# Kernel tuning notes

Hardware: AMD Instinct MI355X
Metric: run time of the kernel (lower is better)

## Reference

```python
import jax, jax.numpy as jnp
import numpy as np

B = 1048576
STATE_DIM, HIDDEN, LATENT = 21, 64, 14
LN_EPS = 1e-5
# index map replicating the torch repeat/cat reconstruction of metric attention (13 -> 21)
EXPAND_IDX = np.array([0, 1, 2, 3, 4, 4, 5, 5, 5, 6, 6, 6, 7, 7, 8, 9, 9, 10, 10, 11, 12])


def setup_inputs() -> dict:
    key = jax.random.key(0)
    ks = jax.random.split(key, 20)

    def w(k, shape, fan_in):
        return (jax.random.uniform(k, shape, jnp.float32, -1.0, 1.0) / np.sqrt(fan_in))

    return {
        'state': jax.random.normal(ks[0], (B, STATE_DIM), jnp.float32),
        # encoder
        'W_enc1': w(ks[1], (STATE_DIM, HIDDEN), STATE_DIM),
        'b_enc1': w(ks[2], (HIDDEN,), STATE_DIM),
        'ln_g': jnp.ones((HIDDEN,), jnp.float32),
        'ln_b': jnp.zeros((HIDDEN,), jnp.float32),
        'W_enc2': w(ks[3], (HIDDEN, HIDDEN), HIDDEN),
        'b_enc2': w(ks[4], (HIDDEN,), HIDDEN),
        'W_enc3': w(ks[5], (HIDDEN, LATENT), HIDDEN),
        'b_enc3': w(ks[6], (LATENT,), HIDDEN),
        # decoder
        'W_dec1': w(ks[7], (LATENT, HIDDEN), LATENT),
        'b_dec1': w(ks[8], (HIDDEN,), LATENT),
        'W_dec2': w(ks[9], (HIDDEN, 8), HIDDEN),
        'b_dec2': w(ks[10], (8,), HIDDEN),
        # attention heads
        'W_m': w(ks[11], (STATE_DIM, 13), STATE_DIM),
        'b_m': w(ks[12], (13,), STATE_DIM),
        'W_h': w(ks[13], (STATE_DIM, 6), STATE_DIM),
        'b_h': w(ks[14], (6,), STATE_DIM),
        'W_c': w(ks[15], (STATE_DIM, 4), STATE_DIM),
        'b_c': w(ks[16], (4,), STATE_DIM),
        # learnable head scales (init 1.0 as in torch)
        's_m': jnp.asarray(1.0, jnp.float32),
        's_h': jnp.asarray(1.0, jnp.float32),
        's_c': jnp.asarray(1.0, jnp.float32),
    }


def _normalize(state):
    ns = state
    ns = ns.at[:, 0:2].set(state[:, 0:2] / 3.0)
    ns = ns.at[:, 17].set(state[:, 17] / 2.0)
    ns = ns.at[:, 18].set(state[:, 18] / 4.0)
    ns = ns.at[:, 19].set(jnp.clip(state[:, 19], 0.0, 2.0) / 2.0)
    return ns


def _layernorm(x, g, b):
    mu = jnp.mean(x, axis=-1, keepdims=True)
    var = jnp.mean(jnp.square(x - mu), axis=-1, keepdims=True)
    return (x - mu) / jnp.sqrt(var + LN_EPS) * g + b


def reference(state, W_enc1, b_enc1, ln_g, ln_b, W_enc2, b_enc2, W_enc3, b_enc3,
              W_dec1, b_dec1, W_dec2, b_dec2, W_m, b_m, W_h, b_h, W_c, b_c,
              s_m, s_h, s_c):
    ns = _normalize(state)  # [B, 21]

    metric = jax.nn.softmax(ns @ W_m + b_m, axis=-1) * (jax.nn.sigmoid(s_m) * 2.0)  # [B,13]
    hyp = jax.nn.softmax(ns @ W_h + b_h, axis=-1) * (jax.nn.sigmoid(s_h) * 2.0)      # [B,6]
    curr = jax.nn.softmax(ns @ W_c + b_c, axis=-1) * (jax.nn.sigmoid(s_c) * 2.0)     # [B,4]

    attended = ns * metric[:, EXPAND_IDX]  # [B,21]

    h = jnp.tanh(_layernorm(attended @ W_enc1 + b_enc1, ln_g, ln_b))
    h = jax.nn.relu(h @ W_enc2 + b_enc2)
    latent = h @ W_enc3 + b_enc3  # [B,14]

    d = jax.nn.relu(latent @ W_dec1 + b_dec1)
    corrections = jnp.tanh(d @ W_dec2 + b_dec2)  # [B,8]

    return corrections, latent, metric, hyp, curr
```

## Files before the change

kernel.cpp:

```cpp
#include <hip/hip_runtime.h>

static constexpr int SD = 21, HD = 64, LT = 14;
static constexpr int NFRAG = 40;

typedef _Float16       f16x4  __attribute__((ext_vector_type(4)));
typedef float          f32x4  __attribute__((ext_vector_type(4)));
typedef unsigned       u32x2v __attribute__((ext_vector_type(2)));
typedef unsigned short u16x4v __attribute__((ext_vector_type(4)));
typedef __fp16         pk2    __attribute__((ext_vector_type(2)));

__device__ __forceinline__ float frcp(float x){ return __builtin_amdgcn_rcpf(x); }
__device__ __forceinline__ float frsq(float x){ return __builtin_amdgcn_rsqf(x); }

__device__ __forceinline__ void wave_fence(){
    asm volatile("s_waitcnt lgkmcnt(0)" ::: "memory");
    __builtin_amdgcn_sched_barrier(0);
}

__device__ __forceinline__ unsigned packrtz(float a, float b){
    pk2 h = __builtin_amdgcn_cvt_pkrtz(a, b);
    union { pk2 h; unsigned u; } u; u.h = h; return u.u;
}
__device__ __forceinline__ unsigned short f16bits(float v){
    _Float16 h = (_Float16)v;
    union { _Float16 h; unsigned short s; } u; u.h = h; return u.s;
}
__device__ __forceinline__ float ftanh(float x){
    x = fminf(15.0f, fmaxf(-15.0f, x));
    float e = __expf(2.0f * x);
    return (e - 1.0f) * frcp(e + 1.0f);
}
template<int NN>
__device__ __forceinline__ void softmax_scale(float (&v)[NN], float gate){
    float mx = v[0];
#pragma unroll
    for (int j = 1; j < NN; ++j) mx = fmaxf(mx, v[j]);
    float s = 0.0f;
#pragma unroll
    for (int j = 0; j < NN; ++j){ v[j] = __expf(v[j] - mx); s += v[j]; }
    float r = frcp(s) * gate;
#pragma unroll
    for (int j = 0; j < NN; ++j) v[j] *= r;
}

union Frag2 { u32x2v u2; unsigned u[2]; f16x4 f; };
union FragH { u16x4v uh; f16x4 f; };

__device__ __forceinline__ f32x4 mfma16(f16x4 a, f16x4 b, f32x4 c){
    return __builtin_amdgcn_mfma_f32_16x16x16f16(a, b, c, 0, 0, 0);
}

__device__ __forceinline__ float headsW(const float* Wm, const float* Wh,
                                        const float* Wc, int k, int j){
    if (j < 13) return Wm[k*13 + j];
    if (j < 19) return Wh[k*6 + (j - 13)];
    if (j < 23) return Wc[k*4 + (j - 19)];
    return 0.0f;
}

__global__ void pack_bfrags(const float* __restrict__ W1, const float* __restrict__ W2,
                            const float* __restrict__ W3, const float* __restrict__ Wd1,
                            const float* __restrict__ Wd2,
                            const float* __restrict__ Wm, const float* __restrict__ Wh,
                            const float* __restrict__ Wc, unsigned* __restrict__ ws)
{
    int t = blockIdx.x * blockDim.x + threadIdx.x;
    if (t >= NFRAG * 64) return;
    int fid = t >> 6, lane = t & 63;
    int g = lane >> 4, c = lane & 15;

    if (fid >= 36) {
        int e = fid - 36, ks16 = e >> 1, ct = e & 1;
        int col = ct*16 + c;
#pragma unroll
        for (int j = 0; j < 2; ++j) {
            int k0 = ks16*16 + g*4 + 2*j;
            float a = (k0     < SD && col < 23) ? headsW(Wm, Wh, Wc, k0,   col) : 0.0f;
            float b = (k0 + 1 < SD && col < 23) ? headsW(Wm, Wh, Wc, k0+1, col) : 0.0f;
            ws[fid*128 + lane*2 + j] = packrtz(a, b);
        }
        return;
    }

    const float* W; int ks16, ct, K, Ncol, ld;
    if (fid < 8)       { W = W1;  ks16 = fid >> 2;    ct = fid & 3;  K = 21; Ncol = 64; ld = 64; }
    else if (fid < 24) { int e = fid - 8;
                         W = W2;  ks16 = e >> 2;      ct = e & 3;    K = 64; Ncol = 64; ld = 64; }
    else if (fid < 28) { W = W3;  ks16 = fid - 24;    ct = 0;        K = 64; Ncol = 14; ld = 14; }
    else if (fid < 32) { W = Wd1; ks16 = 0;           ct = fid - 28; K = 14; Ncol = 64; ld = 64; }
    else               { W = Wd2; ks16 = fid - 32;    ct = 0;        K = 64; Ncol = 8;  ld = 8;  }
    int col = ct*16 + c;
#pragma unroll
    for (int j = 0; j < 2; ++j) {
        int k0 = ks16*16 + g*4 + 2*j;
        float a = (k0     < K && col < Ncol) ? W[k0*ld + col]     : 0.0f;
        float b = (k0 + 1 < K && col < Ncol) ? W[(k0+1)*ld + col] : 0.0f;
        ws[fid*128 + lane*2 + j] = packrtz(a, b);
    }
}

__global__ __launch_bounds__(256) void statenet_mfma7(
    const float* __restrict__ state,
    const unsigned* __restrict__ pw,
    const float* __restrict__ b1,
    const float* __restrict__ lng, const float* __restrict__ lnb,
    const float* __restrict__ b2,  const float* __restrict__ b3,
    const float* __restrict__ bd1, const float* __restrict__ bd2,
    const float* __restrict__ bm,  const float* __restrict__ bh,
    const float* __restrict__ bc,
    const float* __restrict__ psm, const float* __restrict__ psh,
    const float* __restrict__ psc,
    float* __restrict__ out, int N)
{
    __shared__ __align__(16) unsigned s_buf[4*1152];
    __shared__ __align__(16) float    s_lg[4*832];

    const int tid = threadIdx.x;
    const int w  = tid >> 6, l = tid & 63;
    const int cl = l & 15,  g = l >> 4;
    const long long rowbase = (long long)blockIdx.x * 128 + w * 32;

    unsigned*       at  = s_buf + w * 1152;
    unsigned short* hb  = reinterpret_cast<unsigned short*>(s_buf) + w * 2304;
    float*          slg = s_lg + w * 832;

    const float bc0 = (cl < 13) ? bm[cl] : bh[cl - 13];
    const float bc1 = (cl < 3) ? bh[cl + 3] : ((cl < 7) ? bc[cl - 3] : 0.0f);

    float ns[SD];
    if (l < 32) {
        const long long row = rowbase + l;
        {
            const float* p = state + row * SD;
#pragma unroll
            for (int k = 0; k < SD; ++k) ns[k] = p[k];
        }
        ns[0]  *= (1.0f / 3.0f);
        ns[1]  *= (1.0f / 3.0f);
        ns[17] *= 0.5f;
        ns[18] *= 0.25f;
        ns[19]  = fminf(fmaxf(ns[19], 0.0f), 2.0f) * 0.5f;

        const int base = l * 36;
#pragma unroll
        for (int kk = 0; kk < 10; ++kk) at[base + kk] = packrtz(ns[2*kk], ns[2*kk+1]);
        at[base + 10] = packrtz(ns[20], 0.0f);
#pragma unroll
        for (int kk = 11; kk < 16; ++kk) at[base + kk] = 0u;
    }
    wave_fence();

    const u32x2v* BF2 = reinterpret_cast<const u32x2v*>(pw);
    const f32x4 vzero = {0.0f, 0.0f, 0.0f, 0.0f};
    {
        Frag2 aN[2][2];
#pragma unroll
        for (int m2 = 0; m2 < 2; ++m2)
#pragma unroll
            for (int ks = 0; ks < 2; ++ks)
                aN[m2][ks].u2 = *reinterpret_cast<const u32x2v*>(&at[(m2*16 + cl)*36 + ks*8 + 2*g]);
        f32x4 hl[2][2];
#pragma unroll
        for (int m2 = 0; m2 < 2; ++m2)
#pragma unroll
            for (int ct = 0; ct < 2; ++ct) hl[m2][ct] = vzero;
#pragma unroll
        for (int ct = 0; ct < 2; ++ct)
#pragma unroll
            for (int ks = 0; ks < 2; ++ks) {
                Frag2 bf; bf.u2 = BF2[(36 + ks*2 + ct)*64 + l];
#pragma unroll
                for (int m2 = 0; m2 < 2; ++m2)
                    hl[m2][ct] = mfma16(aN[m2][ks].f, bf.f, hl[m2][ct]);
            }
#pragma unroll
        for (int m2 = 0; m2 < 2; ++m2)
#pragma unroll
            for (int q = 0; q < 4; ++q) {
                int r = m2*16 + g*4 + q;
                slg[r*26 + cl] = hl[m2][0][q] + bc0;
                if (cl < 8) slg[r*26 + 16 + cl] = hl[m2][1][q] + bc1;
            }
    }
    wave_fence();

    if (l < 32) {
        const long long row = rowbase + l;
        float lg[24];
#pragma unroll
        for (int i = 0; i < 12; ++i) {
            float2 v = *reinterpret_cast<const float2*>(&slg[l*26 + 2*i]);
            lg[2*i] = v.x; lg[2*i+1] = v.y;
        }
        float m[13], hv[6], cv[4];
#pragma unroll
        for (int j = 0; j < 13; ++j) m[j]  = lg[j];
#pragma unroll
        for (int j = 0; j < 6;  ++j) hv[j] = lg[13 + j];
#pragma unroll
        for (int j = 0; j < 4;  ++j) cv[j] = lg[19 + j];

        const float gm = 2.0f * frcp(1.0f + __expf(-psm[0]));
        const float gh = 2.0f * frcp(1.0f + __expf(-psh[0]));
        const float gc = 2.0f * frcp(1.0f + __expf(-psc[0]));
        softmax_scale<13>(m,  gm);
        softmax_scale<6 >(hv, gh);
        softmax_scale<4 >(cv, gc);

        {
            float* pm = out + (long long)22 * N + row * 13;
#pragma unroll
            for (int j = 0; j < 13; ++j) pm[j] = m[j];
            float* ph = out + (long long)35 * N + row * 6;
#pragma unroll
            for (int j = 0; j < 3; ++j)
                reinterpret_cast<float2*>(ph)[j] = make_float2(hv[2*j], hv[2*j+1]);
            float* pc = out + (long long)41 * N + row * 4;
            reinterpret_cast<float4*>(pc)[0] = make_float4(cv[0], cv[1], cv[2], cv[3]);
        }

        constexpr int EIDX[SD] = {0,1,2,3,4,4,5,5,5,6,6,6,7,7,8,9,9,10,10,11,12};
        float atv[SD];
#pragma unroll
        for (int k = 0; k < SD; ++k) atv[k] = ns[k] * m[EIDX[k]];
        const int base = l * 36;
#pragma unroll
        for (int kk = 0; kk < 10; ++kk) at[base + kk] = packrtz(atv[2*kk], atv[2*kk+1]);
        at[base + 10] = packrtz(atv[20], 0.0f);
    }
    wave_fence();

    float b1c[4], b2c[4], bd1c[4], lgc[4], lbc[4];
#pragma unroll
    for (int t2 = 0; t2 < 4; ++t2) {
        int c2 = cl + 16*t2;
        b1c[t2] = b1[c2];  b2c[t2] = b2[c2];  bd1c[t2] = bd1[c2];
        lgc[t2] = lng[c2]; lbc[t2] = lnb[c2];
    }
    const float b3c  = (cl < 14) ? b3[cl]  : 0.0f;
    const float bd2c = (cl < 8)  ? bd2[cl] : 0.0f;

    Frag2 aA[2][2];
#pragma unroll
    for (int m2 = 0; m2 < 2; ++m2)
#pragma unroll
        for (int ks = 0; ks < 2; ++ks)
            aA[m2][ks].u2 = *reinterpret_cast<const u32x2v*>(&at[(m2*16 + cl)*36 + ks*8 + 2*g]);
    wave_fence();

    f32x4 acc[2][4];
#pragma unroll
    for (int m2 = 0; m2 < 2; ++m2)
#pragma unroll
        for (int ct = 0; ct < 4; ++ct) acc[m2][ct] = vzero;
#pragma unroll
    for (int ct = 0; ct < 4; ++ct)
#pragma unroll
        for (int ks = 0; ks < 2; ++ks) {
            Frag2 bf; bf.u2 = BF2[(ks*4 + ct)*64 + l];
#pragma unroll
            for (int m2 = 0; m2 < 2; ++m2)
                acc[m2][ct] = mfma16(aA[m2][ks].f, bf.f, acc[m2][ct]);
        }
#pragma unroll
    for (int m2 = 0; m2 < 2; ++m2) {
        float s[4], ss[4];
#pragma unroll
        for (int q = 0; q < 4; ++q) {
            float v0 = acc[m2][0][q] + b1c[0], v1 = acc[m2][1][q] + b1c[1];
            float v2 = acc[m2][2][q] + b1c[2], v3 = acc[m2][3][q] + b1c[3];
            acc[m2][0][q] = v0; acc[m2][1][q] = v1; acc[m2][2][q] = v2; acc[m2][3][q] = v3;
            s[q]  = v0 + v1 + v2 + v3;
            ss[q] = v0*v0 + v1*v1 + v2*v2 + v3*v3;
        }
#pragma unroll
        for (int q = 0; q < 4; ++q) {
#pragma unroll
            for (int d = 1; d < 16; d <<= 1) {
                s[q]  += __shfl_xor(s[q],  d, 16);
                ss[q] += __shfl_xor(ss[q], d, 16);
            }
        }
#pragma unroll
        for (int q = 0; q < 4; ++q) {
            float mu   = s[q] * (1.0f/64.0f);
            float var  = ss[q] * (1.0f/64.0f) - mu*mu;
            float istd = frsq(var + 1e-5f);
            int r = m2*16 + g*4 + q;
#pragma unroll
            for (int t2 = 0; t2 < 4; ++t2) {
                float v = ftanh(fmaf((acc[m2][t2][q] - mu) * istd, lgc[t2], lbc[t2]));
                hb[r*72 + cl + 16*t2] = f16bits(v);
            }
        }
    }
    wave_fence();

    FragH ah[2][4];
#pragma unroll
    for (int m2 = 0; m2 < 2; ++m2)
#pragma unroll
        for (int ks = 0; ks < 4; ++ks)
            ah[m2][ks].uh = *reinterpret_cast<const u16x4v*>(&hb[(m2*16 + cl)*72 + ks*16 + 4*g]);
    f32x4 a2[2][4];
#pragma unroll
    for (int m2 = 0; m2 < 2; ++m2)
#pragma unroll
        for (int ct = 0; ct < 4; ++ct) a2[m2][ct] = vzero;
#pragma unroll
    for (int ct = 0; ct < 4; ++ct)
#pragma unroll
        for (int ks = 0; ks < 4; ++ks) {
            Frag2 bf; bf.u2 = BF2[(8 + ks*4 + ct)*64 + l];
#pragma unroll
            for (int m2 = 0; m2 < 2; ++m2)
                a2[m2][ct] = mfma16(ah[m2][ks].f, bf.f, a2[m2][ct]);
        }
    wave_fence();
#pragma unroll
    for (int m2 = 0; m2 < 2; ++m2)
#pragma unroll
        for (int q = 0; q < 4; ++q) {
            int r = m2*16 + g*4 + q;
#pragma unroll
            for (int t2 = 0; t2 < 4; ++t2)
                hb[r*72 + cl + 16*t2] = f16bits(fmaxf(a2[m2][t2][q] + b2c[t2], 0.0f));
        }
    wave_fence();

#pragma unroll
    for (int m2 = 0; m2 < 2; ++m2)
#pragma unroll
        for (int ks = 0; ks < 4; ++ks)
            ah[m2][ks].uh = *reinterpret_cast<const u16x4v*>(&hb[(m2*16 + cl)*72 + ks*16 + 4*g]);
    wave_fence();
#pragma unroll
    for (int m2 = 0; m2 < 2; ++m2) {
        f32x4 a3 = vzero;
#pragma unroll
        for (int ks = 0; ks < 4; ++ks) {
            Frag2 bf; bf.u2 = BF2[(24 + ks)*64 + l];
            a3 = mfma16(ah[m2][ks].f, bf.f, a3);
        }
#pragma unroll
        for (int q = 0; q < 4; ++q) {
            float lv = a3[q] + b3c;
            int r = m2*16 + g*4 + q;
            if (cl < 14)
                out[(long long)8 * N + (rowbase + r) * 14 + cl] = lv;
            float pv = __shfl_xor(lv, 1);
            if ((cl & 1) == 0)
                at[r*36 + (cl >> 1)] = packrtz(lv, pv);
        }
    }
    wave_fence();

    Frag2 aD[2];
#pragma unroll
    for (int m2 = 0; m2 < 2; ++m2)
        aD[m2].u2 = *reinterpret_cast<const u32x2v*>(&at[(m2*16 + cl)*36 + 2*g]);
    wave_fence();
    f32x4 ad[2][4];
#pragma unroll
    for (int m2 = 0; m2 < 2; ++m2)
#pragma unroll
        for (int ct = 0; ct < 4; ++ct) ad[m2][ct] = vzero;
#pragma unroll
    for (int ct = 0; ct < 4; ++ct) {
        Frag2 bf; bf.u2 = BF2[(28 + ct)*64 + l];
#pragma unroll
        for (int m2 = 0; m2 < 2; ++m2)
            ad[m2][ct] = mfma16(aD[m2].f, bf.f, ad[m2][ct]);
    }
#pragma unroll
    for (int m2 = 0; m2 < 2; ++m2)
#pragma unroll
        for (int q = 0; q < 4; ++q) {
            int r = m2*16 + g*4 + q;
#pragma unroll
            for (int t2 = 0; t2 < 4; ++t2)
                hb[r*72 + cl + 16*t2] = f16bits(fmaxf(ad[m2][t2][q] + bd1c[t2], 0.0f));
        }
    wave_fence();

#pragma unroll
    for (int m2 = 0; m2 < 2; ++m2)
#pragma unroll
        for (int ks = 0; ks < 4; ++ks)
            ah[m2][ks].uh = *reinterpret_cast<const u16x4v*>(&hb[(m2*16 + cl)*72 + ks*16 + 4*g]);
#pragma unroll
    for (int m2 = 0; m2 < 2; ++m2) {
        f32x4 a5 = vzero;
#pragma unroll
        for (int ks = 0; ks < 4; ++ks) {
            Frag2 bf; bf.u2 = BF2[(32 + ks)*64 + l];
            a5 = mfma16(ah[m2][ks].f, bf.f, a5);
        }
#pragma unroll
        for (int q = 0; q < 4; ++q) {
            if (cl < 8)
                out[(rowbase + m2*16 + g*4 + q) * 8 + cl] = ftanh(a5[q] + bd2c);
        }
    }
}

extern "C" void kernel_launch(void* const* d_in, const int* in_sizes, int n_in,
                              void* d_out, int out_size, void* d_ws, size_t ws_size,
                              hipStream_t stream)
{
    const float* state = (const float*)d_in[0];
    const float* W1   = (const float*)d_in[1];
    const float* b1   = (const float*)d_in[2];
    const float* lng  = (const float*)d_in[3];
    const float* lnb  = (const float*)d_in[4];
    const float* W2   = (const float*)d_in[5];
    const float* b2   = (const float*)d_in[6];
    const float* W3   = (const float*)d_in[7];
    const float* b3   = (const float*)d_in[8];
    const float* Wd1  = (const float*)d_in[9];
    const float* bd1  = (const float*)d_in[10];
    const float* Wd2  = (const float*)d_in[11];
    const float* bd2  = (const float*)d_in[12];
    const float* Wm   = (const float*)d_in[13];
    const float* bm   = (const float*)d_in[14];
    const float* Wh   = (const float*)d_in[15];
    const float* bh   = (const float*)d_in[16];
    const float* Wc   = (const float*)d_in[17];
    const float* bc   = (const float*)d_in[18];
    const float* psm  = (const float*)d_in[19];
    const float* psh  = (const float*)d_in[20];
    const float* psc  = (const float*)d_in[21];

    unsigned* pw = (unsigned*)d_ws;

    hipLaunchKernelGGL(pack_bfrags, dim3((NFRAG*64 + 255)/256), dim3(256), 0, stream,
                       W1, W2, W3, Wd1, Wd2, Wm, Wh, Wc, pw);

    const int N = in_sizes[0] / SD;
    hipLaunchKernelGGL(statenet_mfma7, dim3(N / 128), dim3(256), 0, stream,
                       state, pw, b1, lng, lnb, b2, b3, bd1, bd2,
                       bm, bh, bc, psm, psh, psc,
                       (float*)d_out, N);
}
```

Before: 123.0 us.

## Chain MLP layers through MFMA accumulators via transposed products, dropping LDS staging

Swaps the operand order of each MFMA so it computes the transposed product (weights as A, activations as B). The output fragment of one layer then already has the layout of the B operand for the next layer. Hidden activations are packed to fp16 in registers and fed straight into the next MFMA, which removes the LDS write/read round trips and wave fences between encoder and decoder layers. LayerNorm reductions become two cross-group shuffles, and bias loads and output stores are vectorized. This raises register pressure and moves the head biases into the softmax thread's scalar loop.

```diff
diff --git a/kernel.cpp b/kernel.cpp
--- a/kernel.cpp
+++ b/kernel.cpp
@@ -6,7 +6,6 @@
 typedef _Float16       f16x4  __attribute__((ext_vector_type(4)));
 typedef float          f32x4  __attribute__((ext_vector_type(4)));
 typedef unsigned       u32x2v __attribute__((ext_vector_type(2)));
-typedef unsigned short u16x4v __attribute__((ext_vector_type(4)));
 typedef __fp16         pk2    __attribute__((ext_vector_type(2)));
 
 __device__ __forceinline__ float frcp(float x){ return __builtin_amdgcn_rcpf(x); }
@@ -20,10 +19,6 @@
 __device__ __forceinline__ unsigned packrtz(float a, float b){
     pk2 h = __builtin_amdgcn_cvt_pkrtz(a, b);
     union { pk2 h; unsigned u; } u; u.h = h; return u.u;
-}
-__device__ __forceinline__ unsigned short f16bits(float v){
-    _Float16 h = (_Float16)v;
-    union { _Float16 h; unsigned short s; } u; u.h = h; return u.s;
 }
 __device__ __forceinline__ float ftanh(float x){
     x = fminf(15.0f, fmaxf(-15.0f, x));
@@ -44,7 +39,6 @@
 }
 
 union Frag2 { u32x2v u2; unsigned u[2]; f16x4 f; };
-union FragH { u16x4v uh; f16x4 f; };
 
 __device__ __forceinline__ f32x4 mfma16(f16x4 a, f16x4 b, f32x4 c){
     return __builtin_amdgcn_mfma_f32_16x16x16f16(a, b, c, 0, 0, 0);
@@ -99,7 +93,7 @@
     }
 }
 
-__global__ __launch_bounds__(256) void statenet_mfma7(
+__global__ __launch_bounds__(256) void statenet_mfma8(
     const float* __restrict__ state,
     const unsigned* __restrict__ pw,
     const float* __restrict__ b1,
@@ -112,7 +106,7 @@
     const float* __restrict__ psc,
     float* __restrict__ out, int N)
 {
-    __shared__ __align__(16) unsigned s_buf[4*1152];
+    __shared__ __align__(16) unsigned s_at[4*1152];
     __shared__ __align__(16) float    s_lg[4*832];
 
     const int tid = threadIdx.x;
@@ -120,12 +114,11 @@
     const int cl = l & 15,  g = l >> 4;
     const long long rowbase = (long long)blockIdx.x * 128 + w * 32;
 
-    unsigned*       at  = s_buf + w * 1152;
-    unsigned short* hb  = reinterpret_cast<unsigned short*>(s_buf) + w * 2304;
-    float*          slg = s_lg + w * 832;
-
-    const float bc0 = (cl < 13) ? bm[cl] : bh[cl - 13];
-    const float bc1 = (cl < 3) ? bh[cl + 3] : ((cl < 7) ? bc[cl - 3] : 0.0f);
+    unsigned* at  = s_at + w * 1152;
+    float*    slg = s_lg + w * 832;
+
+    const u32x2v* BF2 = reinterpret_cast<const u32x2v*>(pw);
+    const f32x4 vzero = {0.0f, 0.0f, 0.0f, 0.0f};
 
     float ns[SD];
     if (l < 32) {
@@ -150,8 +143,6 @@
     }
     wave_fence();
 
-    const u32x2v* BF2 = reinterpret_cast<const u32x2v*>(pw);
-    const f32x4 vzero = {0.0f, 0.0f, 0.0f, 0.0f};
     {
         Frag2 aN[2][2];
 #pragma unroll
@@ -161,26 +152,29 @@
                 aN[m2][ks].u2 = *reinterpret_cast<const u32x2v*>(&at[(m2*16 + cl)*36 + ks*8 + 2*g]);
         f32x4 hl[2][2];
 #pragma unroll
-        for (int m2 = 0; m2 < 2; ++m2)
-#pragma unroll
-            for (int ct = 0; ct < 2; ++ct) hl[m2][ct] = vzero;
-#pragma unroll
         for (int ct = 0; ct < 2; ++ct)
 #pragma unroll
+            for (int m2 = 0; m2 < 2; ++m2) hl[ct][m2] = vzero;
+#pragma unroll
+        for (int ct = 0; ct < 2; ++ct)
+#pragma unroll
             for (int ks = 0; ks < 2; ++ks) {
-                Frag2 bf; bf.u2 = BF2[(36 + ks*2 + ct)*64 + l];
+                Frag2 wf; wf.u2 = BF2[(36 + ks*2 + ct)*64 + l];
 #pragma unroll
                 for (int m2 = 0; m2 < 2; ++m2)
-                    hl[m2][ct] = mfma16(aN[m2][ks].f, bf.f, hl[m2][ct]);
+                    hl[ct][m2] = mfma16(wf.f, aN[m2][ks].f, hl[ct][m2]);
             }
 #pragma unroll
-        for (int m2 = 0; m2 < 2; ++m2)
-#pragma unroll
-            for (int q = 0; q < 4; ++q) {
-                int r = m2*16 + g*4 + q;
-                slg[r*26 + cl] = hl[m2][0][q] + bc0;
-                if (cl < 8) slg[r*26 + 16 + cl] = hl[m2][1][q] + bc1;
+        for (int m2 = 0; m2 < 2; ++m2) {
+            float* p0 = &slg[(m2*16 + cl)*26 + 4*g];
+            reinterpret_cast<float2*>(p0)[0] = make_float2(hl[0][m2][0], hl[0][m2][1]);
+            reinterpret_cast<float2*>(p0)[1] = make_float2(hl[0][m2][2], hl[0][m2][3]);
+            if (g < 2) {
+                float* p1 = &slg[(m2*16 + cl)*26 + 16 + 4*g];
+                reinterpret_cast<float2*>(p1)[0] = make_float2(hl[1][m2][0], hl[1][m2][1]);
+                reinterpret_cast<float2*>(p1)[1] = make_float2(hl[1][m2][2], hl[1][m2][3]);
             }
+        }
     }
     wave_fence();
 
@@ -194,11 +188,11 @@
         }
         float m[13], hv[6], cv[4];
 #pragma unroll
-        for (int j = 0; j < 13; ++j) m[j]  = lg[j];
-#pragma unroll
-        for (int j = 0; j < 6;  ++j) hv[j] = lg[13 + j];
-#pragma unroll
-        for (int j = 0; j < 4;  ++j) cv[j] = lg[19 + j];
+        for (int j = 0; j < 13; ++j) m[j]  = lg[j]      + bm[j];
+#pragma unroll
+        for (int j = 0; j < 6;  ++j) hv[j] = lg[13 + j] + bh[j];
+#pragma unroll
+        for (int j = 0; j < 4;  ++j) cv[j] = lg[19 + j] + bc[j];
 
         const float gm = 2.0f * frcp(1.0f + __expf(-psm[0]));
         const float gh = 2.0f * frcp(1.0f + __expf(-psh[0]));
@@ -230,176 +224,172 @@
     }
     wave_fence();
 
-    float b1c[4], b2c[4], bd1c[4], lgc[4], lbc[4];
-#pragma unroll
-    for (int t2 = 0; t2 < 4; ++t2) {
-        int c2 = cl + 16*t2;
-        b1c[t2] = b1[c2];  b2c[t2] = b2[c2];  bd1c[t2] = bd1[c2];
-        lgc[t2] = lng[c2]; lbc[t2] = lnb[c2];
-    }
-    const float b3c  = (cl < 14) ? b3[cl]  : 0.0f;
-    const float bd2c = (cl < 8)  ? bd2[cl] : 0.0f;
-
     Frag2 aA[2][2];
 #pragma unroll
     for (int m2 = 0; m2 < 2; ++m2)
 #pragma unroll
         for (int ks = 0; ks < 2; ++ks)
             aA[m2][ks].u2 = *reinterpret_cast<const u32x2v*>(&at[(m2*16 + cl)*36 + ks*8 + 2*g]);
-    wave_fence();
-
-    f32x4 acc[2][4];
-#pragma unroll
-    for (int m2 = 0; m2 < 2; ++m2)
-#pragma unroll
-        for (int ct = 0; ct < 4; ++ct) acc[m2][ct] = vzero;
-#pragma unroll
-    for (int ct = 0; ct < 4; ++ct)
+
+    f32x4 D1[4][2];
+#pragma unroll
+    for (int f = 0; f < 4; ++f)
+#pragma unroll
+        for (int m2 = 0; m2 < 2; ++m2) D1[f][m2] = vzero;
+#pragma unroll
+    for (int f = 0; f < 4; ++f)
 #pragma unroll
         for (int ks = 0; ks < 2; ++ks) {
-            Frag2 bf; bf.u2 = BF2[(ks*4 + ct)*64 + l];
+            Frag2 wf; wf.u2 = BF2[(ks*4 + f)*64 + l];
 #pragma unroll
             for (int m2 = 0; m2 < 2; ++m2)
-                acc[m2][ct] = mfma16(aA[m2][ks].f, bf.f, acc[m2][ct]);
-        }
+                D1[f][m2] = mfma16(wf.f, aA[m2][ks].f, D1[f][m2]);
+        }
+
+    float4 b1q[4], lgq[4], lbq[4];
+#pragma unroll
+    for (int f = 0; f < 4; ++f) {
+        b1q[f] = *reinterpret_cast<const float4*>(&b1[f*16 + 4*g]);
+        lgq[f] = *reinterpret_cast<const float4*>(&lng[f*16 + 4*g]);
+        lbq[f] = *reinterpret_cast<const float4*>(&lnb[f*16 + 4*g]);
+    }
+
+    Frag2 B1[2][4];
 #pragma unroll
     for (int m2 = 0; m2 < 2; ++m2) {
-        float s[4], ss[4];
-#pragma unroll
-        for (int q = 0; q < 4; ++q) {
-            float v0 = acc[m2][0][q] + b1c[0], v1 = acc[m2][1][q] + b1c[1];
-            float v2 = acc[m2][2][q] + b1c[2], v3 = acc[m2][3][q] + b1c[3];
-            acc[m2][0][q] = v0; acc[m2][1][q] = v1; acc[m2][2][q] = v2; acc[m2][3][q] = v3;
-            s[q]  = v0 + v1 + v2 + v3;
-            ss[q] = v0*v0 + v1*v1 + v2*v2 + v3*v3;
-        }
-#pragma unroll
-        for (int q = 0; q < 4; ++q) {
-#pragma unroll
-            for (int d = 1; d < 16; d <<= 1) {
-                s[q]  += __shfl_xor(s[q],  d, 16);
-                ss[q] += __shfl_xor(ss[q], d, 16);
+        float s = 0.0f, ss = 0.0f;
+#pragma unroll
+        for (int f = 0; f < 4; ++f) {
+            float bb[4] = {b1q[f].x, b1q[f].y, b1q[f].z, b1q[f].w};
+#pragma unroll
+            for (int q = 0; q < 4; ++q) {
+                float v = D1[f][m2][q] + bb[q];
+                D1[f][m2][q] = v;
+                s += v; ss = fmaf(v, v, ss);
             }
         }
-#pragma unroll
-        for (int q = 0; q < 4; ++q) {
-            float mu   = s[q] * (1.0f/64.0f);
-            float var  = ss[q] * (1.0f/64.0f) - mu*mu;
-            float istd = frsq(var + 1e-5f);
-            int r = m2*16 + g*4 + q;
-#pragma unroll
-            for (int t2 = 0; t2 < 4; ++t2) {
-                float v = ftanh(fmaf((acc[m2][t2][q] - mu) * istd, lgc[t2], lbc[t2]));
-                hb[r*72 + cl + 16*t2] = f16bits(v);
-            }
-        }
-    }
-    wave_fence();
-
-    FragH ah[2][4];
-#pragma unroll
-    for (int m2 = 0; m2 < 2; ++m2)
-#pragma unroll
-        for (int ks = 0; ks < 4; ++ks)
-            ah[m2][ks].uh = *reinterpret_cast<const u16x4v*>(&hb[(m2*16 + cl)*72 + ks*16 + 4*g]);
-    f32x4 a2[2][4];
-#pragma unroll
-    for (int m2 = 0; m2 < 2; ++m2)
-#pragma unroll
-        for (int ct = 0; ct < 4; ++ct) a2[m2][ct] = vzero;
-#pragma unroll
-    for (int ct = 0; ct < 4; ++ct)
-#pragma unroll
-        for (int ks = 0; ks < 4; ++ks) {
-            Frag2 bf; bf.u2 = BF2[(8 + ks*4 + ct)*64 + l];
+        s  += __shfl_xor(s, 16);  s  += __shfl_xor(s, 32);
+        ss += __shfl_xor(ss, 16); ss += __shfl_xor(ss, 32);
+        float mu   = s * (1.0f/64.0f);
+        float var  = ss * (1.0f/64.0f) - mu*mu;
+        float istd = frsq(var + 1e-5f);
+#pragma unroll
+        for (int f = 0; f < 4; ++f) {
+            float gg[4] = {lgq[f].x, lgq[f].y, lgq[f].z, lgq[f].w};
+            float be[4] = {lbq[f].x, lbq[f].y, lbq[f].z, lbq[f].w};
+            float t0 = ftanh(fmaf((D1[f][m2][0] - mu) * istd, gg[0], be[0]));
+            float t1 = ftanh(fmaf((D1[f][m2][1] - mu) * istd, gg[1], be[1]));
+            float t2 = ftanh(fmaf((D1[f][m2][2] - mu) * istd, gg[2], be[2]));
+            float t3 = ftanh(fmaf((D1[f][m2][3] - mu) * istd, gg[3], be[3]));
+            B1[m2][f].u[0] = packrtz(t0, t1);
+            B1[m2][f].u[1] = packrtz(t2, t3);
+        }
+    }
+
+    f32x4 D2[4][2];
+#pragma unroll
+    for (int f2 = 0; f2 < 4; ++f2)
+#pragma unroll
+        for (int m2 = 0; m2 < 2; ++m2) D2[f2][m2] = vzero;
+#pragma unroll
+    for (int f2 = 0; f2 < 4; ++f2)
+#pragma unroll
+        for (int f = 0; f < 4; ++f) {
+            Frag2 wf; wf.u2 = BF2[(8 + f*4 + f2)*64 + l];
 #pragma unroll
             for (int m2 = 0; m2 < 2; ++m2)
-                a2[m2][ct] = mfma16(ah[m2][ks].f, bf.f, a2[m2][ct]);
-        }
-    wave_fence();
-#pragma unroll
-    for (int m2 = 0; m2 < 2; ++m2)
-#pragma unroll
-        for (int q = 0; q < 4; ++q) {
-            int r = m2*16 + g*4 + q;
-#pragma unroll
-            for (int t2 = 0; t2 < 4; ++t2)
-                hb[r*72 + cl + 16*t2] = f16bits(fmaxf(a2[m2][t2][q] + b2c[t2], 0.0f));
-        }
-    wave_fence();
-
-#pragma unroll
-    for (int m2 = 0; m2 < 2; ++m2)
-#pragma unroll
-        for (int ks = 0; ks < 4; ++ks)
-            ah[m2][ks].uh = *reinterpret_cast<const u16x4v*>(&hb[(m2*16 + cl)*72 + ks*16 + 4*g]);
-    wave_fence();
+                D2[f2][m2] = mfma16(wf.f, B1[m2][f].f, D2[f2][m2]);
+        }
+    Frag2 B2[2][4];
+#pragma unroll
+    for (int f2 = 0; f2 < 4; ++f2) {
+        float4 bq = *reinterpret_cast<const float4*>(&b2[f2*16 + 4*g]);
+        float bb[4] = {bq.x, bq.y, bq.z, bq.w};
+#pragma unroll
+        for (int m2 = 0; m2 < 2; ++m2) {
+            float t0 = fmaxf(D2[f2][m2][0] + bb[0], 0.0f);
+            float t1 = fmaxf(D2[f2][m2][1] + bb[1], 0.0f);
+            float t2 = fmaxf(D2[f2][m2][2] + bb[2], 0.0f);
+            float t3 = fmaxf(D2[f2][m2][3] + bb[3], 0.0f);
+            B2[m2][f2].u[0] = packrtz(t0, t1);
+            B2[m2][f2].u[1] = packrtz(t2, t3);
+        }
+    }
+
+    float b3v[4];
+#pragma unroll
+    for (int q = 0; q < 4; ++q) {
+        int j = 4*g + q;
+        b3v[q] = (j < LT) ? b3[j] : 0.0f;
+    }
+    Frag2 B3[2];
 #pragma unroll
     for (int m2 = 0; m2 < 2; ++m2) {
         f32x4 a3 = vzero;
 #pragma unroll
-        for (int ks = 0; ks < 4; ++ks) {
-            Frag2 bf; bf.u2 = BF2[(24 + ks)*64 + l];
-            a3 = mfma16(ah[m2][ks].f, bf.f, a3);
-        }
-#pragma unroll
-        for (int q = 0; q < 4; ++q) {
-            float lv = a3[q] + b3c;
-            int r = m2*16 + g*4 + q;
-            if (cl < 14)
-                out[(long long)8 * N + (rowbase + r) * 14 + cl] = lv;
-            float pv = __shfl_xor(lv, 1);
-            if ((cl & 1) == 0)
-                at[r*36 + (cl >> 1)] = packrtz(lv, pv);
-        }
-    }
-    wave_fence();
-
-    Frag2 aD[2];
-#pragma unroll
-    for (int m2 = 0; m2 < 2; ++m2)
-        aD[m2].u2 = *reinterpret_cast<const u32x2v*>(&at[(m2*16 + cl)*36 + 2*g]);
-    wave_fence();
-    f32x4 ad[2][4];
-#pragma unroll
-    for (int m2 = 0; m2 < 2; ++m2)
-#pragma unroll
-        for (int ct = 0; ct < 4; ++ct) ad[m2][ct] = vzero;
-#pragma unroll
-    for (int ct = 0; ct < 4; ++ct) {
-        Frag2 bf; bf.u2 = BF2[(28 + ct)*64 + l];
+        for (int f = 0; f < 4; ++f) {
+            Frag2 wf; wf.u2 = BF2[(24 + f)*64 + l];
+            a3 = mfma16(wf.f, B2[m2][f].f, a3);
+        }
+        float lv[4];
+#pragma unroll
+        for (int q = 0; q < 4; ++q)
+            lv[q] = (4*g + q < LT) ? (a3[q] + b3v[q]) : 0.0f;
+        {
+            float* pl = out + (long long)8 * N + (rowbase + m2*16 + cl) * 14 + 4*g;
+            if (g < 3) {
+                reinterpret_cast<float2*>(pl)[0] = make_float2(lv[0], lv[1]);
+                reinterpret_cast<float2*>(pl)[1] = make_float2(lv[2], lv[3]);
+            } else {
+                reinterpret_cast<float2*>(pl)[0] = make_float2(lv[0], lv[1]);
+            }
+        }
+        B3[m2].u[0] = packrtz(lv[0], lv[1]);
+        B3[m2].u[1] = packrtz(lv[2], lv[3]);
+    }
+
+    f32x4 D4[4][2];
+#pragma unroll
+    for (int f = 0; f < 4; ++f)
+#pragma unroll
+        for (int m2 = 0; m2 < 2; ++m2) D4[f][m2] = vzero;
+#pragma unroll
+    for (int f = 0; f < 4; ++f) {
+        Frag2 wf; wf.u2 = BF2[(28 + f)*64 + l];
 #pragma unroll
         for (int m2 = 0; m2 < 2; ++m2)
-            ad[m2][ct] = mfma16(aD[m2].f, bf.f, ad[m2][ct]);
-    }
-#pragma unroll
-    for (int m2 = 0; m2 < 2; ++m2)
-#pragma unroll
-        for (int q = 0; q < 4; ++q) {
-            int r = m2*16 + g*4 + q;
-#pragma unroll
-            for (int t2 = 0; t2 < 4; ++t2)
-                hb[r*72 + cl + 16*t2] = f16bits(fmaxf(ad[m2][t2][q] + bd1c[t2], 0.0f));
-        }
-    wave_fence();
-
-#pragma unroll
-    for (int m2 = 0; m2 < 2; ++m2)
-#pragma unroll
-        for (int ks = 0; ks < 4; ++ks)
-            ah[m2][ks].uh = *reinterpret_cast<const u16x4v*>(&hb[(m2*16 + cl)*72 + ks*16 + 4*g]);
+            D4[f][m2] = mfma16(wf.f, B3[m2].f, D4[f][m2]);
+    }
+    Frag2 B4[2][4];
+#pragma unroll
+    for (int f = 0; f < 4; ++f) {
+        float4 bq = *reinterpret_cast<const float4*>(&bd1[f*16 + 4*g]);
+        float bb[4] = {bq.x, bq.y, bq.z, bq.w};
+#pragma unroll
+        for (int m2 = 0; m2 < 2; ++m2) {
+            float t0 = fmaxf(D4[f][m2][0] + bb[0], 0.0f);
+            float t1 = fmaxf(D4[f][m2][1] + bb[1], 0.0f);
+            float t2 = fmaxf(D4[f][m2][2] + bb[2], 0.0f);
+            float t3 = fmaxf(D4[f][m2][3] + bb[3], 0.0f);
+            B4[m2][f].u[0] = packrtz(t0, t1);
+            B4[m2][f].u[1] = packrtz(t2, t3);
+        }
+    }
+
 #pragma unroll
     for (int m2 = 0; m2 < 2; ++m2) {
         f32x4 a5 = vzero;
 #pragma unroll
-        for (int ks = 0; ks < 4; ++ks) {
-            Frag2 bf; bf.u2 = BF2[(32 + ks)*64 + l];
-            a5 = mfma16(ah[m2][ks].f, bf.f, a5);
-        }
-#pragma unroll
-        for (int q = 0; q < 4; ++q) {
-            if (cl < 8)
-                out[(rowbase + m2*16 + g*4 + q) * 8 + cl] = ftanh(a5[q] + bd2c);
+        for (int f = 0; f < 4; ++f) {
+            Frag2 wf; wf.u2 = BF2[(32 + f)*64 + l];
+            a5 = mfma16(wf.f, B4[m2][f].f, a5);
+        }
+        if (g < 2) {
+            float4 bq = *reinterpret_cast<const float4*>(&bd2[4*g]);
+            float* pc = out + (rowbase + m2*16 + cl) * 8 + 4*g;
+            reinterpret_cast<float4*>(pc)[0] =
+                make_float4(ftanh(a5[0] + bq.x), ftanh(a5[1] + bq.y),
+                            ftanh(a5[2] + bq.z), ftanh(a5[3] + bq.w));
         }
     }
 }
@@ -437,7 +427,7 @@
                        W1, W2, W3, Wd1, Wd2, Wm, Wh, Wc, pw);
 
     const int N = in_sizes[0] / SD;
-    hipLaunchKernelGGL(statenet_mfma7, dim3(N / 128), dim3(256), 0, stream,
+    hipLaunchKernelGGL(statenet_mfma8, dim3(N / 128), dim3(256), 0, stream,
                        state, pw, b1, lng, lnb, b2, b3, bd1, bd2,
                        bm, bh, bc, psm, psh, psc,
                        (float*)d_out, N);
```

After: 123.5 us. Within noise of the previous version (+0.4%).
